# Performance work log

Hardware: AMD Instinct MI355X
Metric: run time of the kernel (lower is better)

Reference implementation:

```python
import jax, jax.numpy as jnp
import numpy as np

L, D, H, IMG, P, B, E = 12, 768, 12, 224, 16, 32, 512
HD = D // H            # 64
FF = 4 * D             # 3072
SEQ = (IMG // P) ** 2 + 1  # 197


def _ln(x, w, b, eps=1e-5):
    m = x.mean(-1, keepdims=True)
    v = jnp.mean((x - m) ** 2, axis=-1, keepdims=True)
    return (x - m) * jax.lax.rsqrt(v + eps) * w + b


def setup_inputs() -> dict:
    key = jax.random.key(0)
    ks = jax.random.split(key, 10)
    r = lambda k, shape, s=0.02: (jax.random.normal(k, shape, jnp.float32) * s)
    return {
        'image': jax.random.normal(ks[0], (B, 3, IMG, IMG), jnp.float32),
        'conv_w': r(ks[1], (D, 3, P, P)),
        'cls_emb': r(ks[2], (D,)),
        'pos_emb': r(ks[3], (SEQ, D)),
        'ln_pre_w': jnp.ones((D,), jnp.float32), 'ln_pre_b': jnp.zeros((D,), jnp.float32),
        'ln1_w': jnp.ones((L, D), jnp.float32), 'ln1_b': jnp.zeros((L, D), jnp.float32),
        'qkv_w': r(ks[4], (L, 3 * D, D)), 'qkv_b': jnp.zeros((L, 3 * D), jnp.float32),
        'out_w': r(ks[5], (L, D, D)), 'out_b': jnp.zeros((L, D), jnp.float32),
        'ln2_w': jnp.ones((L, D), jnp.float32), 'ln2_b': jnp.zeros((L, D), jnp.float32),
        'fc_w': r(ks[6], (L, FF, D)), 'fc_b': jnp.zeros((L, FF), jnp.float32),
        'pr_w': r(ks[7], (L, D, FF)), 'pr_b': jnp.zeros((L, D), jnp.float32),
        'ln_post_w': jnp.ones((D,), jnp.float32), 'ln_post_b': jnp.zeros((D,), jnp.float32),
        'proj': r(ks[8], (D, E)),
    }


def reference(image, conv_w, cls_emb, pos_emb, ln_pre_w, ln_pre_b,
              ln1_w, ln1_b, qkv_w, qkv_b, out_w, out_b,
              ln2_w, ln2_b, fc_w, fc_b, pr_w, pr_b,
              ln_post_w, ln_post_b, proj):
    # patchify: conv stride=kernel=patch, no bias -> [B, D, 14, 14]
    x = jax.lax.conv_general_dilated(image, conv_w, (P, P), 'VALID',
                                     dimension_numbers=('NCHW', 'OIHW', 'NCHW'))
    x = x.reshape(B, D, -1).transpose(0, 2, 1)               # [B, 196, D]
    cls = jnp.broadcast_to(cls_emb, (B, 1, D))
    x = jnp.concatenate([cls, x], axis=1) + pos_emb          # [B, SEQ, D]
    x = _ln(x, ln_pre_w, ln_pre_b)
    x = x.transpose(1, 0, 2)                                  # [SEQ, B, D]
    scale = 1.0 / np.sqrt(HD).astype(np.float32)

    def step(x, p):
        l1w, l1b, qw, qb, ow, ob, l2w, l2b, fw, fb, pw, pb = p
        h = _ln(x, l1w, l1b)
        qkv = h @ qw.T + qb                                    # [SEQ, B, 3D]
        q, k, v = jnp.split(qkv, 3, axis=-1)
        heads = lambda t: t.reshape(SEQ, B * H, HD).transpose(1, 0, 2)  # [B*H, SEQ, HD]
        q = heads(q) * scale
        k = heads(k)
        v = heads(v)
        a = jax.nn.softmax(jnp.einsum('nsh,nth->nst', q, k), axis=-1)   # [B*H, SEQ, SEQ]
        o = jnp.einsum('nst,nth->nsh', a, v)                  # [B*H, SEQ, HD]
        o = o.transpose(1, 0, 2).reshape(SEQ, B, D)
        x = x + (o @ ow.T + ob)
        h = _ln(x, l2w, l2b)
        h = jax.nn.gelu(h @ fw.T + fb, approximate=False)      # torch nn.GELU (exact)
        x = x + (h @ pw.T + pb)
        return x, None

    x, _ = jax.lax.scan(step, x, (ln1_w, ln1_b, qkv_w, qkv_b, out_w, out_b,
                                  ln2_w, ln2_b, fc_w, fc_b, pr_w, pr_b))
    x = x.transpose(1, 0, 2)                                   # [B, SEQ, D]
    cls_tok = _ln(x[:, 0, :], ln_post_w, ln_post_b)
    feats = cls_tok @ proj                                     # [B, E]
    return feats / jnp.linalg.norm(feats, axis=-1, keepdims=True)
```

## Files before the change

kernel.cpp:

```cpp
#include <hip/hip_runtime.h>
#include <stdint.h>

#define SEQ 197
#define NB 32
#define NH 12
#define NTOK (SEQ*NB)
#define MPAD 6400
#define NPATCH 6272

typedef unsigned short u16;
typedef unsigned int u32;
typedef __attribute__((ext_vector_type(8))) short bv8;
typedef __attribute__((ext_vector_type(4))) float f32x4;

__device__ __forceinline__ u16 f2bf(float f){
  u32 u = __float_as_uint(f);
  u = (u + 0x7fffu + ((u >> 16) & 1u)) >> 16;
  return (u16)u;
}
__device__ __forceinline__ float bf2f(u16 h){ return __uint_as_float(((u32)h) << 16); }

#if defined(__has_builtin)
#if __has_builtin(__builtin_amdgcn_global_load_lds)
#define HAS_GLLDS 1
#endif
#endif

__device__ __forceinline__ void gl_lds16(const void* g, void* l){
#ifdef HAS_GLLDS
  __builtin_amdgcn_global_load_lds(
      (const __attribute__((address_space(1))) void*)(uintptr_t)g,
      (__attribute__((address_space(3))) void*)(u32)(uintptr_t)l, 16, 0, 0);
#else
  int lane = threadIdx.x & 63;
  uint4 v = *(const uint4*)((const char*)g);
  *(uint4*)((char*)l + lane*16) = v;
#endif
}

__device__ __forceinline__ void red2(float& a, float& b){
  #pragma unroll
  for (int o = 32; o > 0; o >>= 1){ a += __shfl_down(a, o); b += __shfl_down(b, o); }
  __shared__ float red[8];
  int w = threadIdx.x >> 6, ln = threadIdx.x & 63;
  if (ln == 0){ red[w] = a; red[4 + w] = b; }
  __syncthreads();
  a = red[0] + red[1] + red[2] + red[3];
  b = red[4] + red[5] + red[6] + red[7];
}

__global__ __launch_bounds__(256) void cvt_k(const float* __restrict__ src, u16* __restrict__ dst, int n4){
  int i = blockIdx.x * 256 + threadIdx.x;
  if (i >= n4) return;
  float4 f = ((const float4*)src)[i];
  u32 lo = (u32)f2bf(f.x) | ((u32)f2bf(f.y) << 16);
  u32 hi = (u32)f2bf(f.z) | ((u32)f2bf(f.w) << 16);
  ((uint2*)dst)[i] = make_uint2(lo, hi);
}

__global__ __launch_bounds__(256) void im2col_k(const float* __restrict__ img, u16* __restrict__ Ap){
  int gid = blockIdx.x * 256 + threadIdx.x;
  int row = gid / 768, k = gid - row * 768;
  int b = row / 196, p = row - b * 196;
  int pr = p / 14, pc = p - pr * 14;
  int c = k >> 8, r = k & 255;
  int ph = r >> 4, pw = r & 15;
  size_t src = ((size_t)(b * 3 + c) * 224 + (pr * 16 + ph)) * 224 + (pc * 16 + pw);
  Ap[gid] = f2bf(img[src]);
}

template<int EPI>
__global__ __launch_bounds__(256, 2)
void gemm_sw(const u16* __restrict__ A, const u16* __restrict__ Bw,
             const float* __restrict__ bias, float* __restrict__ Cf,
             u16* __restrict__ Cb, int N, int K, int Mreal,
             int RM, int RN, int tmT, int tnT)
{
  __shared__ __align__(16) u16 sA[128 * 64];
  __shared__ __align__(16) u16 sB[128 * 64];
  const int xcd = blockIdx.x & 7, pos = blockIdx.x >> 3;
  const int xm = xcd >> 1, xn = xcd & 1;
  const int tm = xm * RM + pos / RN;
  const int tn = xn * RN + pos % RN;
  if (tm >= tmT || tn >= tnT) return;

  const int tid = threadIdx.x;
  const int lane = tid & 63, wave = tid >> 6;
  const int wm = wave >> 1, wn = wave & 1;
  const int lr = lane & 15, g = lane >> 4, g4 = g * 4;
  const int KT = K >> 6;

  const int srow = lane >> 3;
  const int sch = (lane & 7) ^ srow;
  const u16* aB[4]; const u16* bB[4];
  u16* lA[4]; u16* lB[4];
  #pragma unroll
  for (int j = 0; j < 4; j++){
    int rr = wave * 32 + j * 8;
    aB[j] = A  + (size_t)(tm * 128 + rr + srow) * K + sch * 8;
    bB[j] = Bw + (size_t)(tn * 128 + rr + srow) * K + sch * 8;
    lA[j] = sA + rr * 64;
    lB[j] = sB + rr * 64;
  }

  f32x4 acc[4][4] = {};

  for (int kt = 0; kt < KT; ++kt){
    __syncthreads();
    #pragma unroll
    for (int j = 0; j < 4; j++) gl_lds16(aB[j] + (size_t)kt * 64, lA[j]);
    #pragma unroll
    for (int j = 0; j < 4; j++) gl_lds16(bB[j] + (size_t)kt * 64, lB[j]);
    __syncthreads();
    #pragma unroll
    for (int kk = 0; kk < 2; kk++){
      bv8 af[4], bf[4];
      #pragma unroll
      for (int mi = 0; mi < 4; mi++){
        int row = wm * 64 + mi * 16 + lr;
        af[mi] = *(const bv8*)((const char*)sA + row * 128 + ((kk * 64 + g * 16) ^ ((row & 7) << 4)));
      }
      #pragma unroll
      for (int ni = 0; ni < 4; ni++){
        int row = wn * 64 + ni * 16 + lr;
        bf[ni] = *(const bv8*)((const char*)sB + row * 128 + ((kk * 64 + g * 16) ^ ((row & 7) << 4)));
      }
      #pragma unroll
      for (int mi = 0; mi < 4; mi++)
        #pragma unroll
        for (int ni = 0; ni < 4; ni++)
          acc[mi][ni] = __builtin_amdgcn_mfma_f32_16x16x32_bf16(af[mi], bf[ni], acc[mi][ni], 0, 0, 0);
    }
  }

  if (EPI == 1 || EPI == 3){
    __syncthreads();
    u16* sC = sA;
    #pragma unroll
    for (int mi = 0; mi < 4; mi++){
      #pragma unroll
      for (int ni = 0; ni < 4; ni++){
        int bcol = wn * 64 + ni * 16 + lr;
        float bvs = bias[tn * 128 + bcol];
        #pragma unroll
        for (int j = 0; j < 4; j++){
          int brow = wm * 64 + mi * 16 + g4 + j;
          float v = acc[mi][ni][j] + bvs;
          if (EPI == 3) v = 0.5f * v * (1.f + erff(v * 0.70710678118654752f));
          *(u16*)((char*)sC + brow * 256 + ((bcol * 2) ^ ((brow & 7) << 4))) = f2bf(v);
        }
      }
    }
    __syncthreads();
    #pragma unroll
    for (int c = 0; c < 8; c++){
      int off = c * 4096 + tid * 16;
      int row = off >> 8;
      int colb = off & 255;
      uint4 v = *(const uint4*)((const char*)sC + row * 256 + (colb ^ ((row & 7) << 4)));
      *(uint4*)((char*)(Cb + (size_t)(tm * 128 + row) * N + tn * 128) + colb) = v;
    }
  } else {
    #pragma unroll
    for (int ni = 0; ni < 4; ni++){
      int col = tn * 128 + wn * 64 + ni * 16 + lr;
      float bvs = (EPI != 0) ? bias[col] : 0.f;
      #pragma unroll
      for (int mi = 0; mi < 4; mi++){
        int row0 = tm * 128 + wm * 64 + mi * 16 + g4;
        #pragma unroll
        for (int j = 0; j < 4; j++){
          int row = row0 + j;
          if (row < Mreal){
            float v = acc[mi][ni][j] + bvs;
            size_t idx = (size_t)row * N + col;
            if (EPI == 0) Cf[idx] = v;
            else          Cf[idx] += v;
          }
        }
      }
    }
  }
}

template<int EPI>
__global__ __launch_bounds__(256, 2)
void gemm_2ph(const u16* __restrict__ A, const u16* __restrict__ Bw,
              const float* __restrict__ bias, float* __restrict__ Cf,
              u16* __restrict__ Cb, int N, int K, int Mreal,
              int RM, int RN, int tmT, int tnT)
{
  __shared__ __align__(16) u16 sA0[128 * 64];
  __shared__ __align__(16) u16 sB0[128 * 64];
  __shared__ __align__(16) u16 sA1[128 * 64];
  __shared__ __align__(16) u16 sB1[128 * 64];
  const int xcd = blockIdx.x & 7, pos = blockIdx.x >> 3;
  const int xm = xcd >> 1, xn = xcd & 1;
  const int tm = xm * RM + pos / RN;
  const int tn = xn * RN + pos % RN;
  if (tm >= tmT || tn >= tnT) return;

  const int tid = threadIdx.x;
  const int lane = tid & 63, wave = tid >> 6;
  const int wm = wave >> 1, wn = wave & 1;
  const int lr = lane & 15, g = lane >> 4, g4 = g * 4;
  const int KT = K >> 6;

  const int srow = lane >> 3;
  const int sch = (lane & 7) ^ srow;
  const u16* aB[4]; const u16* bB[4];
  #pragma unroll
  for (int j = 0; j < 4; j++){
    int rr = wave * 32 + j * 8;
    aB[j] = A  + (size_t)(tm * 128 + rr + srow) * K + sch * 8;
    bB[j] = Bw + (size_t)(tn * 128 + rr + srow) * K + sch * 8;
  }

  f32x4 acc[4][4] = {};

  auto stage = [&](int kt, u16* dA, u16* dB){
    #pragma unroll
    for (int j = 0; j < 4; j++)
      gl_lds16(aB[j] + (size_t)kt * 64, dA + (wave * 32 + j * 8) * 64);
    #pragma unroll
    for (int j = 0; j < 4; j++)
      gl_lds16(bB[j] + (size_t)kt * 64, dB + (wave * 32 + j * 8) * 64);
  };
  auto tile = [&](const u16* sA, const u16* sB, u16* dA, u16* dB, int ktNext, bool doStage, bool last){
    if (last) asm volatile("s_waitcnt vmcnt(0)" ::: "memory");
    else      asm volatile("s_waitcnt vmcnt(8)" ::: "memory");
    __builtin_amdgcn_s_barrier();
    bv8 af[4][2], bf[4][2];
    #pragma unroll
    for (int mi = 0; mi < 4; mi++){
      int row = wm * 64 + mi * 16 + lr;
      #pragma unroll
      for (int kk = 0; kk < 2; kk++)
        af[mi][kk] = *(const bv8*)((const char*)sA + row * 128 + ((kk * 64 + g * 16) ^ ((row & 7) << 4)));
    }
    #pragma unroll
    for (int ni = 0; ni < 4; ni++){
      int row = wn * 64 + ni * 16 + lr;
      #pragma unroll
      for (int kk = 0; kk < 2; kk++)
        bf[ni][kk] = *(const bv8*)((const char*)sB + row * 128 + ((kk * 64 + g * 16) ^ ((row & 7) << 4)));
    }
    asm volatile("s_waitcnt lgkmcnt(0)" ::: "memory");
    __builtin_amdgcn_s_barrier();
    if (doStage) stage(ktNext, dA, dB);
    __builtin_amdgcn_s_setprio(1);
    #pragma unroll
    for (int kk = 0; kk < 2; kk++)
      #pragma unroll
      for (int mi = 0; mi < 4; mi++)
        #pragma unroll
        for (int ni = 0; ni < 4; ni++)
          acc[mi][ni] = __builtin_amdgcn_mfma_f32_16x16x32_bf16(af[mi][kk], bf[ni][kk], acc[mi][ni], 0, 0, 0);
    __builtin_amdgcn_s_setprio(0);
  };

  stage(0, sA0, sB0);
  stage(1, sA1, sB1);
  int t = 0;
  for (; t + 2 < KT; t += 2){
    tile(sA0, sB0, sA0, sB0, t + 2, true,  false);
    tile(sA1, sB1, sA1, sB1, t + 3, true,  false);
  }
  tile(sA0, sB0, sA0, sB0, 0, false, false);
  tile(sA1, sB1, sA1, sB1, 0, false, true);

  if (EPI == 1 || EPI == 3){
    __syncthreads();
    #pragma unroll
    for (int mi = 0; mi < 4; mi++){
      #pragma unroll
      for (int ni = 0; ni < 4; ni++){
        int bcol = wn * 64 + ni * 16 + lr;
        float bvs = bias[tn * 128 + bcol];
        #pragma unroll
        for (int j = 0; j < 4; j++){
          int brow = wm * 64 + mi * 16 + g4 + j;
          float v = acc[mi][ni][j] + bvs;
          if (EPI == 3) v = 0.5f * v * (1.f + erff(v * 0.70710678118654752f));
          char* base = (char*)(brow < 64 ? sA0 : sB0);
          *(u16*)(base + (brow & 63) * 256 + ((bcol * 2) ^ ((brow & 7) << 4))) = f2bf(v);
        }
      }
    }
    __syncthreads();
    #pragma unroll
    for (int c = 0; c < 8; c++){
      int off = c * 4096 + tid * 16;
      int row = off >> 8;
      int colb = off & 255;
      const char* base = (const char*)(row < 64 ? sA0 : sB0);
      uint4 v = *(const uint4*)(base + (row & 63) * 256 + (colb ^ ((row & 7) << 4)));
      *(uint4*)((char*)(Cb + (size_t)(tm * 128 + row) * N + tn * 128) + colb) = v;
    }
  } else {
    #pragma unroll
    for (int ni = 0; ni < 4; ni++){
      int col = tn * 128 + wn * 64 + ni * 16 + lr;
      float bvs = (EPI != 0) ? bias[col] : 0.f;
      #pragma unroll
      for (int mi = 0; mi < 4; mi++){
        int row0 = tm * 128 + wm * 64 + mi * 16 + g4;
        #pragma unroll
        for (int j = 0; j < 4; j++){
          int row = row0 + j;
          if (row < Mreal){
            float v = acc[mi][ni][j] + bvs;
            size_t idx = (size_t)row * N + col;
            if (EPI == 0) Cf[idx] = v;
            else          Cf[idx] += v;
          }
        }
      }
    }
  }
}

__global__ __launch_bounds__(256, 2) void attn_k(const u16* __restrict__ qkv, u16* __restrict__ o_out){
  __shared__ __align__(16) u16 sK[256 * 64];
  __shared__ __align__(16) u16 sVT[64 * 256];
  __shared__ __align__(16) u16 sP[4 * 32 * 64];
  const int bh2 = blockIdx.x;
  const int bh = bh2 >> 1, half = bh2 & 1;
  const int b = bh / NH, h = bh - b * NH;
  const int tid = threadIdx.x;
  const int lane = tid & 63, wave = tid >> 6;
  const int lr = lane & 15, g = lane >> 4;
  const int g4 = g * 4;
  const int wb = half * 128 + wave * 32;
  const u16* kbase = qkv + (size_t)b * SEQ * 2304 + h * 64 + 768;
  const u16* vbase = kbase + 768;

  bv8 qf[2][2];
  #pragma unroll
  for (int qt = 0; qt < 2; qt++){
    int q = wb + qt * 16 + lr; if (q > 196) q = 196;
    const u16* qr = qkv + (size_t)(b * SEQ + q) * 2304 + h * 64;
    #pragma unroll
    for (int kc = 0; kc < 2; kc++)
      qf[qt][kc] = *(const bv8*)(qr + kc * 32 + g * 8);
  }

  for (int i = tid; i < 197 * 32; i += 256){
    int r = i >> 5, c = i & 31;
    u32 kv_ = *(const u32*)(kbase + (size_t)r * 2304 + c * 2);
    *(u32*)((char*)sK + ((r * 128 + c * 4) ^ ((r & 7) << 4))) = kv_;
    u32 vv = *(const u32*)(vbase + (size_t)r * 2304 + c * 2);
    int hd0 = c * 2, hd1 = c * 2 + 1;
    *(u16*)((char*)sVT + ((hd0 * 512 + r * 2) ^ ((hd0 & 7) << 4))) = (u16)(vv & 0xffff);
    *(u16*)((char*)sVT + ((hd1 * 512 + r * 2) ^ ((hd1 & 7) << 4))) = (u16)(vv >> 16);
  }
  for (int i = tid; i < 59 * 32; i += 256){
    int r = 197 + (i >> 5), c = i & 31;
    *(u32*)((char*)sK + (r * 128 + c * 4)) = 0;
  }
  for (int i = tid; i < 59 * 64; i += 256){
    int kv = 197 + (i >> 6), hd = i & 63;
    *(u16*)((char*)sVT + ((hd * 512 + kv * 2) ^ ((hd & 7) << 4))) = 0;
  }
  __syncthreads();

  f32x4 acc_o[2][4] = {};
  float m_[2] = {-1e30f, -1e30f};
  float l_[2] = {0.f, 0.f};
  u16* sPw = sP + wave * 2048;

  for (int ch = 0; ch < 4; ++ch){
    f32x4 st[4][2] = {};
    #pragma unroll
    for (int kc = 0; kc < 2; kc++){
      bv8 kf[4];
      #pragma unroll
      for (int kvt = 0; kvt < 4; kvt++){
        int row = ch * 64 + kvt * 16 + lr;
        kf[kvt] = *(const bv8*)((const char*)sK + ((row * 128 + kc * 64 + g * 16) ^ ((row & 7) << 4)));
      }
      #pragma unroll
      for (int kvt = 0; kvt < 4; kvt++)
        #pragma unroll
        for (int qt = 0; qt < 2; qt++)
          st[kvt][qt] = __builtin_amdgcn_mfma_f32_16x16x32_bf16(kf[kvt], qf[qt][kc], st[kvt][qt], 0, 0, 0);
    }
    float fac[2];
    #pragma unroll
    for (int qt = 0; qt < 2; qt++){
      float mx = -1e30f;
      #pragma unroll
      for (int kvt = 0; kvt < 4; kvt++)
        #pragma unroll
        for (int j = 0; j < 4; j++){
          int kvg = ch * 64 + kvt * 16 + g4 + j;
          float s = st[kvt][qt][j] * 0.125f;
          s = (kvg < 197) ? s : -1e30f;
          st[kvt][qt][j] = s;
          mx = fmaxf(mx, s);
        }
      mx = fmaxf(mx, __shfl_xor(mx, 16));
      mx = fmaxf(mx, __shfl_xor(mx, 32));
      float nm = fmaxf(m_[qt], mx);
      fac[qt] = __expf(m_[qt] - nm);
      m_[qt] = nm;
      float ls = 0.f;
      #pragma unroll
      for (int kvt = 0; kvt < 4; kvt++)
        #pragma unroll
        for (int j = 0; j < 4; j++){
          float p = __expf(st[kvt][qt][j] - nm);
          st[kvt][qt][j] = p;
          ls += p;
        }
      ls += __shfl_xor(ls, 16);
      ls += __shfl_xor(ls, 32);
      l_[qt] = l_[qt] * fac[qt] + ls;
    }
    #pragma unroll
    for (int qt = 0; qt < 2; qt++)
      #pragma unroll
      for (int j = 0; j < 4; j++){
        float fj = __shfl(fac[qt], (lane & 48) | (g4 + j));
        #pragma unroll
        for (int nt = 0; nt < 4; nt++) acc_o[qt][nt][j] *= fj;
      }
    #pragma unroll
    for (int qt = 0; qt < 2; qt++){
      int row = qt * 16 + lr;
      #pragma unroll
      for (int kvt = 0; kvt < 4; kvt++){
        uint2 pk;
        pk.x = (u32)f2bf(st[kvt][qt][0]) | ((u32)f2bf(st[kvt][qt][1]) << 16);
        pk.y = (u32)f2bf(st[kvt][qt][2]) | ((u32)f2bf(st[kvt][qt][3]) << 16);
        *(uint2*)((char*)sPw + ((row * 128 + kvt * 32 + g * 8) ^ ((row & 7) << 4))) = pk;
      }
    }
    #pragma unroll
    for (int kc = 0; kc < 2; kc++){
      bv8 pa[2], vb[4];
      #pragma unroll
      for (int qt = 0; qt < 2; qt++){
        int row = qt * 16 + lr;
        pa[qt] = *(const bv8*)((const char*)sPw + ((row * 128 + kc * 64 + g * 16) ^ ((row & 7) << 4)));
      }
      #pragma unroll
      for (int nt = 0; nt < 4; nt++){
        int hd = nt * 16 + lr;
        vb[nt] = *(const bv8*)((const char*)sVT + ((hd * 512 + ch * 128 + kc * 64 + g * 16) ^ ((hd & 7) << 4)));
      }
      #pragma unroll
      for (int qt = 0; qt < 2; qt++)
        #pragma unroll
        for (int nt = 0; nt < 4; nt++)
          acc_o[qt][nt] = __builtin_amdgcn_mfma_f32_16x16x32_bf16(pa[qt], vb[nt], acc_o[qt][nt], 0, 0, 0);
    }
  }

  #pragma unroll
  for (int qt = 0; qt < 2; qt++)
    #pragma unroll
    for (int j = 0; j < 4; j++){
      float lj = __shfl(l_[qt], (lane & 48) | (g4 + j));
      float rl = 1.f / lj;
      int row = wb + qt * 16 + g4 + j;
      if (row < 197){
        u16* dst = o_out + (size_t)(b * SEQ + row) * 768 + h * 64;
        #pragma unroll
        for (int nt = 0; nt < 4; nt++)
          dst[nt * 16 + lr] = f2bf(acc_o[qt][nt][j] * rl);
      }
    }
}

__global__ __launch_bounds__(256) void embed_ln_k(const float* __restrict__ patch, const float* __restrict__ cls,
    const float* __restrict__ pos, const float* __restrict__ w, const float* __restrict__ bb, float* __restrict__ x)
{
  int t = blockIdx.x;
  int b = t / SEQ, s = t - b * SEQ;
  int tid = threadIdx.x;
  float v[3];
  #pragma unroll
  for (int i = 0; i < 3; i++){
    int d = tid + i * 256;
    float base = (s == 0) ? cls[d] : patch[(size_t)(b * 196 + s - 1) * 768 + d];
    v[i] = base + pos[s * 768 + d];
  }
  float sm = v[0] + v[1] + v[2];
  float sq = v[0]*v[0] + v[1]*v[1] + v[2]*v[2];
  red2(sm, sq);
  float m = sm * (1.f / 768.f);
  float rs = rsqrtf(sq * (1.f / 768.f) - m * m + 1e-5f);
  #pragma unroll
  for (int i = 0; i < 3; i++){
    int d = tid + i * 256;
    x[(size_t)t * 768 + d] = (v[i] - m) * rs * w[d] + bb[d];
  }
}

__global__ __launch_bounds__(256) void ln_bf16_k(const float* __restrict__ x, const float* __restrict__ w,
    const float* __restrict__ bb, u16* __restrict__ h)
{
  int t = blockIdx.x, tid = threadIdx.x;
  const float* xr = x + (size_t)t * 768;
  float v[3];
  #pragma unroll
  for (int i = 0; i < 3; i++) v[i] = xr[tid + i * 256];
  float sm = v[0] + v[1] + v[2];
  float sq = v[0]*v[0] + v[1]*v[1] + v[2]*v[2];
  red2(sm, sq);
  float m = sm * (1.f / 768.f);
  float rs = rsqrtf(sq * (1.f / 768.f) - m * m + 1e-5f);
  #pragma unroll
  for (int i = 0; i < 3; i++){
    int d = tid + i * 256;
    h[(size_t)t * 768 + d] = f2bf((v[i] - m) * rs * w[d] + bb[d]);
  }
}

__global__ __launch_bounds__(256) void ln_cls_k(const float* __restrict__ x, const float* __restrict__ w,
    const float* __restrict__ bb, float* __restrict__ cls)
{
  int b = blockIdx.x, tid = threadIdx.x;
  const float* xr = x + (size_t)b * SEQ * 768;
  float v[3];
  #pragma unroll
  for (int i = 0; i < 3; i++) v[i] = xr[tid + i * 256];
  float sm = v[0] + v[1] + v[2];
  float sq = v[0]*v[0] + v[1]*v[1] + v[2]*v[2];
  red2(sm, sq);
  float m = sm * (1.f / 768.f);
  float rs = rsqrtf(sq * (1.f / 768.f) - m * m + 1e-5f);
  #pragma unroll
  for (int i = 0; i < 3; i++){
    int d = tid + i * 256;
    cls[b * 768 + d] = (v[i] - m) * rs * w[d] + bb[d];
  }
}

__global__ __launch_bounds__(256) void proj_k(const float* __restrict__ cls, const float* __restrict__ P,
                                              float* __restrict__ feats){
  int gid = blockIdx.x * 256 + threadIdx.x;
  int b = gid >> 9, e = gid & 511;
  const float* c = cls + b * 768;
  float a0 = 0, a1 = 0, a2 = 0, a3 = 0;
  for (int d = 0; d < 768; d += 4){
    a0 += c[d]     * P[(size_t)d * 512 + e];
    a1 += c[d + 1] * P[(size_t)(d + 1) * 512 + e];
    a2 += c[d + 2] * P[(size_t)(d + 2) * 512 + e];
    a3 += c[d + 3] * P[(size_t)(d + 3) * 512 + e];
  }
  feats[gid] = (a0 + a1) + (a2 + a3);
}

__global__ __launch_bounds__(256) void norm_k(const float* __restrict__ feats, float* __restrict__ out){
  int b = blockIdx.x, tid = threadIdx.x;
  float v0 = feats[b * 512 + tid], v1 = feats[b * 512 + 256 + tid];
  float sq = v0 * v0 + v1 * v1, dummy = 0.f;
  red2(sq, dummy);
  float inv = 1.f / sqrtf(sq);
  out[b * 512 + tid] = v0 * inv;
  out[b * 512 + 256 + tid] = v1 * inv;
}

extern "C" void kernel_launch(void* const* d_in, const int* in_sizes, int n_in,
                              void* d_out, int out_size, void* d_ws, size_t ws_size,
                              hipStream_t stream)
{
  const float* image   = (const float*)d_in[0];
  const float* conv_w  = (const float*)d_in[1];
  const float* cls_emb = (const float*)d_in[2];
  const float* pos_emb = (const float*)d_in[3];
  const float* lnprew  = (const float*)d_in[4];
  const float* lnpreb  = (const float*)d_in[5];
  const float* ln1w    = (const float*)d_in[6];
  const float* ln1b    = (const float*)d_in[7];
  const float* qkvw    = (const float*)d_in[8];
  const float* qkvb    = (const float*)d_in[9];
  const float* outw    = (const float*)d_in[10];
  const float* outb    = (const float*)d_in[11];
  const float* ln2w    = (const float*)d_in[12];
  const float* ln2b    = (const float*)d_in[13];
  const float* fcw     = (const float*)d_in[14];
  const float* fcb     = (const float*)d_in[15];
  const float* prw     = (const float*)d_in[16];
  const float* prb     = (const float*)d_in[17];
  const float* lnpostw = (const float*)d_in[18];
  const float* lnpostb = (const float*)d_in[19];
  const float* proj    = (const float*)d_in[20];
  (void)in_sizes; (void)n_in; (void)out_size;

  const size_t QW = (size_t)2304 * 768, OW = (size_t)768 * 768;
  const size_t FW = (size_t)3072 * 768, PW = (size_t)768 * 3072;
  const size_t CW = (size_t)768 * 768;

  char* p = (char*)d_ws;
  auto alloc = [&](size_t bytes)->char*{ char* r = p; p += (bytes + 255) & ~(size_t)255; return r; };
  float* x     = (float*)alloc((size_t)MPAD * 768 * 4);
  u16*   h     = (u16*)  alloc((size_t)MPAD * 768 * 2);
  u16*   qkvB  = (u16*)  alloc((size_t)MPAD * 2304 * 2);
  u16*   attno = (u16*)  alloc((size_t)MPAD * 768 * 2);
  u16*   ffh   = (u16*)  alloc((size_t)MPAD * 3072 * 2);
  u16*   Ap    = (u16*)  alloc((size_t)NPATCH * 768 * 2);
  float* patch = (float*)alloc((size_t)NPATCH * 768 * 4);
  float* clsb  = (float*)alloc((size_t)32 * 768 * 4);
  float* feats = (float*)alloc((size_t)32 * 512 * 4);
  u16*   cwb   = (u16*)  alloc(CW * 2);
  size_t base_used = (size_t)(p - (char*)d_ws);
  size_t full_need = (QW + OW + FW + PW) * 12 * 2;
  bool full = (base_used + full_need + 4096 <= ws_size);

  u16 *wq = nullptr, *wo = nullptr, *wf = nullptr, *wp = nullptr;
  u16 *sq_ = nullptr, *so_ = nullptr, *sf_ = nullptr, *sp_ = nullptr;
  if (full){
    wq = (u16*)alloc(QW * 12 * 2); wo = (u16*)alloc(OW * 12 * 2);
    wf = (u16*)alloc(FW * 12 * 2); wp = (u16*)alloc(PW * 12 * 2);
  } else {
    sq_ = (u16*)alloc(QW * 2); so_ = (u16*)alloc(OW * 2);
    sf_ = (u16*)alloc(FW * 2); sp_ = (u16*)alloc(PW * 2);
  }
  if ((size_t)(p - (char*)d_ws) > ws_size) return;

  { int n4 = (int)(CW / 4); cvt_k<<<(n4 + 255) / 256, 256, 0, stream>>>(conv_w, cwb, n4); }
  if (full){
    int n4;
    n4 = (int)(QW * 12 / 4); cvt_k<<<(n4 + 255) / 256, 256, 0, stream>>>(qkvw, wq, n4);
    n4 = (int)(OW * 12 / 4); cvt_k<<<(n4 + 255) / 256, 256, 0, stream>>>(outw, wo, n4);
    n4 = (int)(FW * 12 / 4); cvt_k<<<(n4 + 255) / 256, 256, 0, stream>>>(fcw,  wf, n4);
    n4 = (int)(PW * 12 / 4); cvt_k<<<(n4 + 255) / 256, 256, 0, stream>>>(prw,  wp, n4);
  }

  im2col_k<<<(NPATCH * 768) / 256, 256, 0, stream>>>(image, Ap);
  gemm_sw<0><<<8 * 13 * 3, 256, 0, stream>>>(Ap, cwb, nullptr, patch, nullptr, 768, 768, NPATCH, 13, 3, 49, 6);
  embed_ln_k<<<NTOK, 256, 0, stream>>>(patch, cls_emb, pos_emb, lnprew, lnpreb, x);

  for (int l = 0; l < 12; l++){
    const u16 *WQ, *WO, *WF, *WP;
    if (full){
      WQ = wq + (size_t)l * QW; WO = wo + (size_t)l * OW;
      WF = wf + (size_t)l * FW; WP = wp + (size_t)l * PW;
    } else {
      int n4;
      n4 = (int)(QW / 4); cvt_k<<<(n4 + 255) / 256, 256, 0, stream>>>(qkvw + (size_t)l * QW, sq_, n4);
      n4 = (int)(OW / 4); cvt_k<<<(n4 + 255) / 256, 256, 0, stream>>>(outw + (size_t)l * OW, so_, n4);
      n4 = (int)(FW / 4); cvt_k<<<(n4 + 255) / 256, 256, 0, stream>>>(fcw  + (size_t)l * FW, sf_, n4);
      n4 = (int)(PW / 4); cvt_k<<<(n4 + 255) / 256, 256, 0, stream>>>(prw  + (size_t)l * PW, sp_, n4);
      WQ = sq_; WO = so_; WF = sf_; WP = sp_;
    }
    ln_bf16_k<<<NTOK, 256, 0, stream>>>(x, ln1w + l * 768, ln1b + l * 768, h);
    gemm_sw<1><<<8 * 13 * 9, 256, 0, stream>>>(h, WQ, qkvb + l * 2304, nullptr, qkvB, 2304, 768, NTOK, 13, 9, 50, 18);
    attn_k<<<NB * NH * 2, 256, 0, stream>>>(qkvB, attno);
    gemm_sw<2><<<8 * 13 * 3, 256, 0, stream>>>(attno, WO, outb + l * 768, x, nullptr, 768, 768, NTOK, 13, 3, 50, 6);
    ln_bf16_k<<<NTOK, 256, 0, stream>>>(x, ln2w + l * 768, ln2b + l * 768, h);
    gemm_sw<3><<<8 * 13 * 12, 256, 0, stream>>>(h, WF, fcb + l * 3072, nullptr, ffh, 3072, 768, NTOK, 13, 12, 50, 24);
    gemm_2ph<2><<<8 * 13 * 3, 256, 0, stream>>>(ffh, WP, prb + l * 768, x, nullptr, 768, 3072, NTOK, 13, 3, 50, 6);
  }

  ln_cls_k<<<NB, 256, 0, stream>>>(x, lnpostw, lnpostb, clsb);
  proj_k<<<(NB * 512) / 256, 256, 0, stream>>>(clsb, proj, feats);
  norm_k<<<NB, 256, 0, stream>>>(feats, (float*)d_out);
}
```

Before: 2.738 ms.

## Add double-buffered K=32 GEMM kernel for QKV, out-proj and FC layers

Introduces gemm_p32, a GEMM that stages 32-wide K slices into two LDS buffers with async global-to-LDS loads. Each step issues the prefetch of tile t+2 before running the MFMAs on the current tile. It replaces the single-buffer gemm_sw for the QKV, output-projection and FC1 GEMMs, aiming to hide load latency and cut LDS footprint so more blocks fit per CU. The bf16 epilogue now staging-writes across the four small buffers, and gemm_sw and gemm_2ph are reduced to the fp32 store epilogue only. The cost is more barriers per unit of K work, since each step covers only K=32.

Result: slower. 2.912 ms (+6.3%).

```diff
diff --git a/kernel.cpp b/kernel.cpp
--- a/kernel.cpp
+++ b/kernel.cpp
@@ -133,9 +133,114 @@
     }
   }
 
+  #pragma unroll
+  for (int ni = 0; ni < 4; ni++){
+    int col = tn * 128 + wn * 64 + ni * 16 + lr;
+    float bvs = (EPI != 0) ? bias[col] : 0.f;
+    #pragma unroll
+    for (int mi = 0; mi < 4; mi++){
+      int row0 = tm * 128 + wm * 64 + mi * 16 + g4;
+      #pragma unroll
+      for (int j = 0; j < 4; j++){
+        int row = row0 + j;
+        if (row < Mreal){
+          float v = acc[mi][ni][j] + bvs;
+          size_t idx = (size_t)row * N + col;
+          if (EPI == 0) Cf[idx] = v;
+          else          Cf[idx] += v;
+        }
+      }
+    }
+  }
+}
+
+template<int EPI>
+__global__ __launch_bounds__(256, 2)
+void gemm_p32(const u16* __restrict__ A, const u16* __restrict__ Bw,
+              const float* __restrict__ bias, float* __restrict__ Cf,
+              u16* __restrict__ Cb, int N, int K, int Mreal,
+              int RM, int RN, int tmT, int tnT)
+{
+  __shared__ __align__(16) u16 sA0[4096];
+  __shared__ __align__(16) u16 sB0[4096];
+  __shared__ __align__(16) u16 sA1[4096];
+  __shared__ __align__(16) u16 sB1[4096];
+  const int xcd = blockIdx.x & 7, pos = blockIdx.x >> 3;
+  const int xm = xcd >> 1, xn = xcd & 1;
+  const int tm = xm * RM + pos / RN;
+  const int tn = xn * RN + pos % RN;
+  if (tm >= tmT || tn >= tnT) return;
+
+  const int tid = threadIdx.x;
+  const int lane = tid & 63, wave = tid >> 6;
+  const int wm = wave >> 1, wn = wave & 1;
+  const int lr = lane & 15, g = lane >> 4, g4 = g * 4;
+  const int KT = K >> 5;
+
+  const int lr8 = lane >> 3;
+  const u16* aS[2]; const u16* bS[2]; int lbase[2];
+  #pragma unroll
+  for (int j = 0; j < 2; j++){
+    int rr8 = wave * 16 + j * 8;
+    int ldsrow = rr8 + lr8;
+    int c_log = (lane & 7) ^ (ldsrow & 7);
+    int trow = ldsrow * 2 + (c_log >> 2);
+    int koff = (c_log & 3) * 8;
+    aS[j] = A  + (size_t)(tm * 128 + trow) * K + koff;
+    bS[j] = Bw + (size_t)(tn * 128 + trow) * K + koff;
+    lbase[j] = rr8 * 64;
+  }
+
+  f32x4 acc[4][4] = {};
+
+  auto stage = [&](int kt, u16* dA, u16* dB){
+    #pragma unroll
+    for (int j = 0; j < 2; j++) gl_lds16(aS[j] + kt * 32, dA + lbase[j]);
+    #pragma unroll
+    for (int j = 0; j < 2; j++) gl_lds16(bS[j] + kt * 32, dB + lbase[j]);
+  };
+  auto step = [&](const u16* sAc, const u16* sBc, u16* dA, u16* dB,
+                  int ktNext, bool doStage, bool last){
+    if (last) asm volatile("s_waitcnt vmcnt(0)" ::: "memory");
+    else      asm volatile("s_waitcnt vmcnt(4)" ::: "memory");
+    __builtin_amdgcn_s_barrier();
+    bv8 af[4], bf[4];
+    #pragma unroll
+    for (int mi = 0; mi < 4; mi++){
+      int trow = wm * 64 + mi * 16 + lr;
+      int ldr = trow >> 1;
+      af[mi] = *(const bv8*)((const char*)sAc + ldr * 128 + ((((trow & 1) * 64) + g * 16) ^ ((ldr & 7) << 4)));
+    }
+    #pragma unroll
+    for (int ni = 0; ni < 4; ni++){
+      int trow = wn * 64 + ni * 16 + lr;
+      int ldr = trow >> 1;
+      bf[ni] = *(const bv8*)((const char*)sBc + ldr * 128 + ((((trow & 1) * 64) + g * 16) ^ ((ldr & 7) << 4)));
+    }
+    asm volatile("s_waitcnt lgkmcnt(0)" ::: "memory");
+    __builtin_amdgcn_sched_barrier(0);
+    __builtin_amdgcn_s_barrier();
+    if (doStage) stage(ktNext, dA, dB);
+    __builtin_amdgcn_s_setprio(1);
+    #pragma unroll
+    for (int mi = 0; mi < 4; mi++)
+      #pragma unroll
+      for (int ni = 0; ni < 4; ni++)
+        acc[mi][ni] = __builtin_amdgcn_mfma_f32_16x16x32_bf16(af[mi], bf[ni], acc[mi][ni], 0, 0, 0);
+    __builtin_amdgcn_s_setprio(0);
+  };
+
+  stage(0, sA0, sB0);
+  stage(1, sA1, sB1);
+  for (int t = 0; t < KT - 2; t += 2){
+    step(sA0, sB0, sA0, sB0, t + 2, true, false);
+    step(sA1, sB1, sA1, sB1, t + 3, true, false);
+  }
+  step(sA0, sB0, sA0, sB0, 0, false, false);
+  step(sA1, sB1, sA1, sB1, 0, false, true);
+
   if (EPI == 1 || EPI == 3){
     __syncthreads();
-    u16* sC = sA;
     #pragma unroll
     for (int mi = 0; mi < 4; mi++){
       #pragma unroll
@@ -147,7 +252,9 @@
           int brow = wm * 64 + mi * 16 + g4 + j;
           float v = acc[mi][ni][j] + bvs;
           if (EPI == 3) v = 0.5f * v * (1.f + erff(v * 0.70710678118654752f));
-          *(u16*)((char*)sC + brow * 256 + ((bcol * 2) ^ ((brow & 7) << 4))) = f2bf(v);
+          int sel = brow >> 5;
+          char* base = (char*)(sel == 0 ? sA0 : sel == 1 ? sB0 : sel == 2 ? sA1 : sB1);
+          *(u16*)(base + (brow & 31) * 256 + ((bcol * 2) ^ ((brow & 7) << 4))) = f2bf(v);
         }
       }
     }
@@ -157,7 +264,9 @@
       int off = c * 4096 + tid * 16;
       int row = off >> 8;
       int colb = off & 255;
-      uint4 v = *(const uint4*)((const char*)sC + row * 256 + (colb ^ ((row & 7) << 4)));
+      int sel = row >> 5;
+      const char* base = (const char*)(sel == 0 ? sA0 : sel == 1 ? sB0 : sel == 2 ? sA1 : sB1);
+      uint4 v = *(const uint4*)(base + (row & 31) * 256 + (colb ^ ((row & 7) << 4)));
       *(uint4*)((char*)(Cb + (size_t)(tm * 128 + row) * N + tn * 128) + colb) = v;
     }
   } else {
@@ -269,51 +378,21 @@
   tile(sA0, sB0, sA0, sB0, 0, false, false);
   tile(sA1, sB1, sA1, sB1, 0, false, true);
 
-  if (EPI == 1 || EPI == 3){
-    __syncthreads();
+  #pragma unroll
+  for (int ni = 0; ni < 4; ni++){
+    int col = tn * 128 + wn * 64 + ni * 16 + lr;
+    float bvs = (EPI != 0) ? bias[col] : 0.f;
     #pragma unroll
     for (int mi = 0; mi < 4; mi++){
-      #pragma unroll
-      for (int ni = 0; ni < 4; ni++){
-        int bcol = wn * 64 + ni * 16 + lr;
-        float bvs = bias[tn * 128 + bcol];
-        #pragma unroll
-        for (int j = 0; j < 4; j++){
-          int brow = wm * 64 + mi * 16 + g4 + j;
+      int row0 = tm * 128 + wm * 64 + mi * 16 + g4;
+      #pragma unroll
+      for (int j = 0; j < 4; j++){
+        int row = row0 + j;
+        if (row < Mreal){
           float v = acc[mi][ni][j] + bvs;
-          if (EPI == 3) v = 0.5f * v * (1.f + erff(v * 0.70710678118654752f));
-          char* base = (char*)(brow < 64 ? sA0 : sB0);
-          *(u16*)(base + (brow & 63) * 256 + ((bcol * 2) ^ ((brow & 7) << 4))) = f2bf(v);
-        }
-      }
-    }
-    __syncthreads();
-    #pragma unroll
-    for (int c = 0; c < 8; c++){
-      int off = c * 4096 + tid * 16;
-      int row = off >> 8;
-      int colb = off & 255;
-      const char* base = (const char*)(row < 64 ? sA0 : sB0);
-      uint4 v = *(const uint4*)(base + (row & 63) * 256 + (colb ^ ((row & 7) << 4)));
-      *(uint4*)((char*)(Cb + (size_t)(tm * 128 + row) * N + tn * 128) + colb) = v;
-    }
-  } else {
-    #pragma unroll
-    for (int ni = 0; ni < 4; ni++){
-      int col = tn * 128 + wn * 64 + ni * 16 + lr;
-      float bvs = (EPI != 0) ? bias[col] : 0.f;
-      #pragma unroll
-      for (int mi = 0; mi < 4; mi++){
-        int row0 = tm * 128 + wm * 64 + mi * 16 + g4;
-        #pragma unroll
-        for (int j = 0; j < 4; j++){
-          int row = row0 + j;
-          if (row < Mreal){
-            float v = acc[mi][ni][j] + bvs;
-            size_t idx = (size_t)row * N + col;
-            if (EPI == 0) Cf[idx] = v;
-            else          Cf[idx] += v;
-          }
+          size_t idx = (size_t)row * N + col;
+          if (EPI == 0) Cf[idx] = v;
+          else          Cf[idx] += v;
         }
       }
     }
@@ -648,11 +727,11 @@
       WQ = sq_; WO = so_; WF = sf_; WP = sp_;
     }
     ln_bf16_k<<<NTOK, 256, 0, stream>>>(x, ln1w + l * 768, ln1b + l * 768, h);
-    gemm_sw<1><<<8 * 13 * 9, 256, 0, stream>>>(h, WQ, qkvb + l * 2304, nullptr, qkvB, 2304, 768, NTOK, 13, 9, 50, 18);
+    gemm_p32<1><<<8 * 13 * 9, 256, 0, stream>>>(h, WQ, qkvb + l * 2304, nullptr, qkvB, 2304, 768, NTOK, 13, 9, 50, 18);
     attn_k<<<NB * NH * 2, 256, 0, stream>>>(qkvB, attno);
-    gemm_sw<2><<<8 * 13 * 3, 256, 0, stream>>>(attno, WO, outb + l * 768, x, nullptr, 768, 768, NTOK, 13, 3, 50, 6);
+    gemm_p32<2><<<8 * 13 * 3, 256, 0, stream>>>(attno, WO, outb + l * 768, x, nullptr, 768, 768, NTOK, 13, 3, 50, 6);
     ln_bf16_k<<<NTOK, 256, 0, stream>>>(x, ln2w + l * 768, ln2b + l * 768, h);
-    gemm_sw<3><<<8 * 13 * 12, 256, 0, stream>>>(h, WF, fcb + l * 3072, nullptr, ffh, 3072, 768, NTOK, 13, 12, 50, 24);
+    gemm_p32<3><<<8 * 13 * 12, 256, 0, stream>>>(h, WF, fcb + l * 3072, nullptr, ffh, 3072, 768, NTOK, 13, 12, 50, 24);
     gemm_2ph<2><<<8 * 13 * 3, 256, 0, stream>>>(ffh, WP, prb + l * 768, x, nullptr, 768, 3072, NTOK, 13, 3, 50, 6);
   }
 
```

## Add 256x128-tile, 512-thread GEMM for QKV and FC1 bf16-output projections

Applied to the files above, without the earlier changes.

Adds a gemm_t2 kernel with a 256x128 output tile and 8 waves, so each B-weight tile loaded into LDS is reused across twice as many rows. It replaces gemm_sw for the QKV and FC1 GEMMs. The bf16 epilogue writes its output in two 128-row halves through the A shared buffer. The bf16-store epilogue paths are removed from gemm_sw and gemm_2ph, which now use only the fp32 paths. Risks are lower occupancy from the larger block and a grid of 25 M-tiles reading rows up to 6400, which relies on the padded buffers.

Measured after the change: 3.711 ms. +35.5%, slower.

```diff
diff --git a/kernel.cpp b/kernel.cpp
--- a/kernel.cpp
+++ b/kernel.cpp
@@ -133,52 +133,122 @@
     }
   }
 
-  if (EPI == 1 || EPI == 3){
+  #pragma unroll
+  for (int ni = 0; ni < 4; ni++){
+    int col = tn * 128 + wn * 64 + ni * 16 + lr;
+    float bvs = (EPI != 0) ? bias[col] : 0.f;
+    #pragma unroll
+    for (int mi = 0; mi < 4; mi++){
+      int row0 = tm * 128 + wm * 64 + mi * 16 + g4;
+      #pragma unroll
+      for (int j = 0; j < 4; j++){
+        int row = row0 + j;
+        if (row < Mreal){
+          float v = acc[mi][ni][j] + bvs;
+          size_t idx = (size_t)row * N + col;
+          if (EPI == 0) Cf[idx] = v;
+          else          Cf[idx] += v;
+        }
+      }
+    }
+  }
+}
+
+template<int EPI>
+__global__ __launch_bounds__(512, 2)
+void gemm_t2(const u16* __restrict__ A, const u16* __restrict__ Bw,
+             const float* __restrict__ bias, u16* __restrict__ Cb,
+             int N, int K, int RM, int RN, int tmT, int tnT)
+{
+  __shared__ __align__(16) u16 sA[256 * 64];
+  __shared__ __align__(16) u16 sB[128 * 64];
+  const int xcd = blockIdx.x & 7, pos = blockIdx.x >> 3;
+  const int xm = xcd >> 1, xn = xcd & 1;
+  const int tm = xm * RM + pos / RN;
+  const int tn = xn * RN + pos % RN;
+  if (tm >= tmT || tn >= tnT) return;
+
+  const int tid = threadIdx.x;
+  const int lane = tid & 63, wave = tid >> 6;
+  const int wm = wave >> 1, wn = wave & 1;
+  const int lr = lane & 15, g = lane >> 4, g4 = g * 4;
+  const int KT = K >> 6;
+
+  const int srow = lane >> 3;
+  const int sch = (lane & 7) ^ srow;
+  const u16* aB[4]; const u16* bB[2];
+  u16* lA[4]; u16* lB[2];
+  #pragma unroll
+  for (int j = 0; j < 4; j++){
+    int rr = wave * 32 + j * 8;
+    aB[j] = A + (size_t)(tm * 256 + rr + srow) * K + sch * 8;
+    lA[j] = sA + rr * 64;
+  }
+  #pragma unroll
+  for (int j = 0; j < 2; j++){
+    int rr = wave * 16 + j * 8;
+    bB[j] = Bw + (size_t)(tn * 128 + rr + srow) * K + sch * 8;
+    lB[j] = sB + rr * 64;
+  }
+
+  f32x4 acc[4][4] = {};
+
+  for (int kt = 0; kt < KT; ++kt){
     __syncthreads();
-    u16* sC = sA;
-    #pragma unroll
-    for (int mi = 0; mi < 4; mi++){
+    #pragma unroll
+    for (int j = 0; j < 4; j++) gl_lds16(aB[j] + (size_t)kt * 64, lA[j]);
+    #pragma unroll
+    for (int j = 0; j < 2; j++) gl_lds16(bB[j] + (size_t)kt * 64, lB[j]);
+    __syncthreads();
+    #pragma unroll
+    for (int kk = 0; kk < 2; kk++){
+      bv8 af[4], bf[4];
+      #pragma unroll
+      for (int mi = 0; mi < 4; mi++){
+        int row = wm * 64 + mi * 16 + lr;
+        af[mi] = *(const bv8*)((const char*)sA + row * 128 + ((kk * 64 + g * 16) ^ ((row & 7) << 4)));
+      }
       #pragma unroll
       for (int ni = 0; ni < 4; ni++){
-        int bcol = wn * 64 + ni * 16 + lr;
-        float bvs = bias[tn * 128 + bcol];
-        #pragma unroll
-        for (int j = 0; j < 4; j++){
-          int brow = wm * 64 + mi * 16 + g4 + j;
-          float v = acc[mi][ni][j] + bvs;
-          if (EPI == 3) v = 0.5f * v * (1.f + erff(v * 0.70710678118654752f));
-          *(u16*)((char*)sC + brow * 256 + ((bcol * 2) ^ ((brow & 7) << 4))) = f2bf(v);
+        int row = wn * 64 + ni * 16 + lr;
+        bf[ni] = *(const bv8*)((const char*)sB + row * 128 + ((kk * 64 + g * 16) ^ ((row & 7) << 4)));
+      }
+      #pragma unroll
+      for (int mi = 0; mi < 4; mi++)
+        #pragma unroll
+        for (int ni = 0; ni < 4; ni++)
+          acc[mi][ni] = __builtin_amdgcn_mfma_f32_16x16x32_bf16(af[mi], bf[ni], acc[mi][ni], 0, 0, 0);
+    }
+  }
+
+  #pragma unroll
+  for (int p = 0; p < 2; p++){
+    __syncthreads();
+    if ((wm >> 1) == p){
+      #pragma unroll
+      for (int mi = 0; mi < 4; mi++){
+        #pragma unroll
+        for (int ni = 0; ni < 4; ni++){
+          int bcol = wn * 64 + ni * 16 + lr;
+          float bvs = bias[tn * 128 + bcol];
+          #pragma unroll
+          for (int j = 0; j < 4; j++){
+            int brow = (wm & 1) * 64 + mi * 16 + g4 + j;
+            float v = acc[mi][ni][j] + bvs;
+            if (EPI == 3) v = 0.5f * v * (1.f + erff(v * 0.70710678118654752f));
+            *(u16*)((char*)sA + brow * 256 + ((bcol * 2) ^ ((brow & 7) << 4))) = f2bf(v);
+          }
         }
       }
     }
     __syncthreads();
     #pragma unroll
-    for (int c = 0; c < 8; c++){
-      int off = c * 4096 + tid * 16;
+    for (int c = 0; c < 4; c++){
+      int off = c * 8192 + tid * 16;
       int row = off >> 8;
       int colb = off & 255;
-      uint4 v = *(const uint4*)((const char*)sC + row * 256 + (colb ^ ((row & 7) << 4)));
-      *(uint4*)((char*)(Cb + (size_t)(tm * 128 + row) * N + tn * 128) + colb) = v;
-    }
-  } else {
-    #pragma unroll
-    for (int ni = 0; ni < 4; ni++){
-      int col = tn * 128 + wn * 64 + ni * 16 + lr;
-      float bvs = (EPI != 0) ? bias[col] : 0.f;
-      #pragma unroll
-      for (int mi = 0; mi < 4; mi++){
-        int row0 = tm * 128 + wm * 64 + mi * 16 + g4;
-        #pragma unroll
-        for (int j = 0; j < 4; j++){
-          int row = row0 + j;
-          if (row < Mreal){
-            float v = acc[mi][ni][j] + bvs;
-            size_t idx = (size_t)row * N + col;
-            if (EPI == 0) Cf[idx] = v;
-            else          Cf[idx] += v;
-          }
-        }
-      }
+      uint4 v = *(const uint4*)((const char*)sA + row * 256 + (colb ^ ((row & 7) << 4)));
+      *(uint4*)((char*)(Cb + (size_t)(tm * 256 + p * 128 + row) * N + tn * 128) + colb) = v;
     }
   }
 }
@@ -269,51 +339,21 @@
   tile(sA0, sB0, sA0, sB0, 0, false, false);
   tile(sA1, sB1, sA1, sB1, 0, false, true);
 
-  if (EPI == 1 || EPI == 3){
-    __syncthreads();
+  #pragma unroll
+  for (int ni = 0; ni < 4; ni++){
+    int col = tn * 128 + wn * 64 + ni * 16 + lr;
+    float bvs = (EPI != 0) ? bias[col] : 0.f;
     #pragma unroll
     for (int mi = 0; mi < 4; mi++){
-      #pragma unroll
-      for (int ni = 0; ni < 4; ni++){
-        int bcol = wn * 64 + ni * 16 + lr;
-        float bvs = bias[tn * 128 + bcol];
-        #pragma unroll
-        for (int j = 0; j < 4; j++){
-          int brow = wm * 64 + mi * 16 + g4 + j;
+      int row0 = tm * 128 + wm * 64 + mi * 16 + g4;
+      #pragma unroll
+      for (int j = 0; j < 4; j++){
+        int row = row0 + j;
+        if (row < Mreal){
           float v = acc[mi][ni][j] + bvs;
-          if (EPI == 3) v = 0.5f * v * (1.f + erff(v * 0.70710678118654752f));
-          char* base = (char*)(brow < 64 ? sA0 : sB0);
-          *(u16*)(base + (brow & 63) * 256 + ((bcol * 2) ^ ((brow & 7) << 4))) = f2bf(v);
-        }
-      }
-    }
-    __syncthreads();
-    #pragma unroll
-    for (int c = 0; c < 8; c++){
-      int off = c * 4096 + tid * 16;
-      int row = off >> 8;
-      int colb = off & 255;
-      const char* base = (const char*)(row < 64 ? sA0 : sB0);
-      uint4 v = *(const uint4*)(base + (row & 63) * 256 + (colb ^ ((row & 7) << 4)));
-      *(uint4*)((char*)(Cb + (size_t)(tm * 128 + row) * N + tn * 128) + colb) = v;
-    }
-  } else {
-    #pragma unroll
-    for (int ni = 0; ni < 4; ni++){
-      int col = tn * 128 + wn * 64 + ni * 16 + lr;
-      float bvs = (EPI != 0) ? bias[col] : 0.f;
-      #pragma unroll
-      for (int mi = 0; mi < 4; mi++){
-        int row0 = tm * 128 + wm * 64 + mi * 16 + g4;
-        #pragma unroll
-        for (int j = 0; j < 4; j++){
-          int row = row0 + j;
-          if (row < Mreal){
-            float v = acc[mi][ni][j] + bvs;
-            size_t idx = (size_t)row * N + col;
-            if (EPI == 0) Cf[idx] = v;
-            else          Cf[idx] += v;
-          }
+          size_t idx = (size_t)row * N + col;
+          if (EPI == 0) Cf[idx] = v;
+          else          Cf[idx] += v;
         }
       }
     }
@@ -648,11 +688,11 @@
       WQ = sq_; WO = so_; WF = sf_; WP = sp_;
     }
     ln_bf16_k<<<NTOK, 256, 0, stream>>>(x, ln1w + l * 768, ln1b + l * 768, h);
-    gemm_sw<1><<<8 * 13 * 9, 256, 0, stream>>>(h, WQ, qkvb + l * 2304, nullptr, qkvB, 2304, 768, NTOK, 13, 9, 50, 18);
+    gemm_t2<1><<<8 * 7 * 9, 512, 0, stream>>>(h, WQ, qkvb + l * 2304, qkvB, 2304, 768, 7, 9, 25, 18);
     attn_k<<<NB * NH * 2, 256, 0, stream>>>(qkvB, attno);
     gemm_sw<2><<<8 * 13 * 3, 256, 0, stream>>>(attno, WO, outb + l * 768, x, nullptr, 768, 768, NTOK, 13, 3, 50, 6);
     ln_bf16_k<<<NTOK, 256, 0, stream>>>(x, ln2w + l * 768, ln2b + l * 768, h);
-    gemm_sw<3><<<8 * 13 * 12, 256, 0, stream>>>(h, WF, fcb + l * 3072, nullptr, ffh, 3072, 768, NTOK, 13, 12, 50, 24);
+    gemm_t2<3><<<8 * 7 * 12, 512, 0, stream>>>(h, WF, fcb + l * 3072, ffh, 3072, 768, 7, 12, 25, 24);
     gemm_2ph<2><<<8 * 13 * 3, 256, 0, stream>>>(ffh, WP, prb + l * 768, x, nullptr, 768, 3072, NTOK, 13, 3, 50, 6);
   }
 
```
